# Performance work log

Measured on AMD Instinct MI355X. Metric: run time of the kernel, lower is better.

Reference implementation:

```python
import jax, jax.numpy as jnp
import numpy as np

N, C, H, W = 8, 256, 128, 128
HD = 256          # hidden_depth
FC, FS, CS = 8, 2, 8  # heads_count, fold_size, center_size
EPS_GN = 1e-5


def setup_inputs() -> dict:
    key = jax.random.key(0)
    ks = jax.random.split(key, 8)
    d = {
        'x': jax.random.normal(ks[0], (N, C, H, W), jnp.float32),
        'proj_w': jax.random.normal(ks[1], (2 * HD, C), jnp.float32) * 0.02,
        'proj_b': jnp.zeros((2 * HD,), jnp.float32),
        'merge_w': jax.random.normal(ks[2], (C, HD), jnp.float32) * 0.02,
        'merge_b': jnp.zeros((C,), jnp.float32),
        'alpha': jnp.ones((1,), jnp.float32),
        'beta': jnp.zeros((1,), jnp.float32),
        'g0_w': jnp.ones((C,), jnp.float32),
        'g0_b': jnp.zeros((C,), jnp.float32),
        'mlp_w0': jax.random.normal(ks[3], (2 * C, 2 * C), jnp.float32) * 0.02,
        'mlp_b0': jnp.zeros((2 * C,), jnp.float32),
        'mlp_w1': jax.random.normal(ks[4], (2 * C, C), jnp.float32) * 0.02,
        'mlp_b1': jnp.zeros((C,), jnp.float32),
        'g1_w': jnp.ones((C,), jnp.float32),
        'g1_b': jnp.zeros((C,), jnp.float32),
        'layer_scale': jnp.full((C,), 1e-5, jnp.float32),
    }
    return d


def _group_norm1(x, w, b):
    # GroupNorm(1, C): normalize over (C,H,W) per sample, per-channel affine
    mu = x.mean(axis=(1, 2, 3), keepdims=True)
    var = ((x - mu) ** 2).mean(axis=(1, 2, 3), keepdims=True)
    xn = (x - mu) * jax.lax.rsqrt(var + EPS_GN)
    return xn * w[None, :, None, None] + b[None, :, None, None]


def _l2norm(v):
    return v / jnp.maximum(jnp.linalg.norm(v, axis=-1, keepdims=True), 1e-12)


def _local_cluster(x, proj_w, proj_b, merge_w, merge_b, alpha, beta):
    n = x.shape[0]
    # 1x1 conv proj: C -> 2*HD
    y = jnp.einsum('nchw,oc->nohw', x, proj_w) + proj_b[None, :, None, None]
    c = y.shape[1] // FC              # per-head channels (2*HD/FC)
    h, w = H // FS, W // FS
    # 'n (fc c) (fh h) (fw w) -> (n fc fh fw) c h w'
    y = y.reshape(n, FC, c, FS, h, FS, w).transpose(0, 1, 3, 5, 2, 4, 6)
    y = y.reshape(n * FC * FS * FS, c, h, w)
    m = y.shape[0]
    # adaptive avg pool to CSxCS (h,w divisible by CS -> uniform pooling)
    center = y.reshape(m, c, CS, h // CS, CS, w // CS).mean(axis=(3, 5))
    L, s = h * w, CS * CS
    yf = y.reshape(m, c, L).transpose(0, 2, 1)       # [m, L, c]
    cf = center.reshape(m, c, s).transpose(0, 2, 1)  # [m, s, c]
    cv = c // 2
    x_point, x_value = yf[..., :cv], yf[..., cv:]
    c_point, c_value = cf[..., :cv], cf[..., cv:]
    sim = jnp.einsum('mlc,msc->mls', _l2norm(x_point), _l2norm(c_point))
    sim = jax.nn.sigmoid(alpha * sim + beta)         # [m, L, s]
    vals = sim.max(axis=2)                           # [m, L]
    idx = sim.argmax(axis=2) + s * jnp.arange(m)[:, None]
    vals = vals.reshape(-1)
    idx = idx.reshape(-1)
    xv = x_value.reshape(-1, cv)
    cvv = c_value.reshape(-1, cv)
    xv_aug = jnp.concatenate([xv, jnp.ones((xv.shape[0], 1), xv.dtype)], axis=1)
    cv_aug = jnp.concatenate([cvv, jnp.ones((cvv.shape[0], 1), cvv.dtype)], axis=1)
    # scatter-add weighted points into centers
    nc = cv_aug.at[idx].add(vals[:, None] * xv_aug)
    nc = nc[:, :-1] / nc[:, -1:]
    # gather back
    nx = vals[:, None] * nc[idx]                     # [m*L, cv]
    # '(n fc fh fw h w) c -> n (fc c) (fh h) (fw w)'
    nx = nx.reshape(n, FC, FS, FS, h, w, cv).transpose(0, 1, 6, 2, 4, 3, 5)
    nx = nx.reshape(n, FC * cv, H, W)                # [n, HD, H, W]
    return jnp.einsum('nchw,oc->nohw', nx, merge_w) + merge_b[None, :, None, None]


def reference(x, proj_w, proj_b, merge_w, merge_b, alpha, beta, g0_w, g0_b,
              mlp_w0, mlp_b0, mlp_w1, mlp_b1, g1_w, g1_b, layer_scale):
    new_x = _local_cluster(x, proj_w, proj_b, merge_w, merge_b, alpha, beta)
    new_x = _group_norm1(new_x, g0_w, g0_b)
    t = jnp.concatenate([x, new_x], axis=1)          # [n, 2C, H, W]
    t = t.transpose(0, 2, 3, 1)                      # NHWC
    t = jax.nn.gelu(t @ mlp_w0 + mlp_b0, approximate=False)
    t = t @ mlp_w1 + mlp_b1
    t = t.transpose(0, 3, 1, 2)                      # NCHW
    t = _group_norm1(t, g1_w, g1_b)
    t = t * layer_scale[None, :, None, None]
    return t + x
```

## Files before the change

kernel.cpp:

```cpp
#include <hip/hip_runtime.h>
#include <math.h>

#define PIX   16384
#define NB    8
#define CIN   256

typedef __attribute__((ext_vector_type(8))) short    short8;
typedef __attribute__((ext_vector_type(4))) float    f32x4;
typedef __attribute__((ext_vector_type(4))) unsigned short us4;
typedef __attribute__((ext_vector_type(8))) unsigned short us8;

__device__ __forceinline__ float bf2f(unsigned short h) {
  return __uint_as_float(((unsigned int)h) << 16);
}
__device__ __forceinline__ unsigned short f2bf(float f) {
  unsigned int u = __float_as_uint(f);
  return (unsigned short)((u + 0x7FFFu + ((u >> 16) & 1u)) >> 16);
}
__device__ __forceinline__ float gelu_f(float v) {
  return 0.5f * v * (1.f + erff(v * 0.70710678118654752f));
}

__device__ __forceinline__ float rowmax16(float v) {
  v = fmaxf(v, __uint_as_float(__builtin_amdgcn_update_dpp(
        __float_as_uint(v), __float_as_uint(v), 0x121, 0xF, 0xF, false)));
  v = fmaxf(v, __uint_as_float(__builtin_amdgcn_update_dpp(
        __float_as_uint(v), __float_as_uint(v), 0x122, 0xF, 0xF, false)));
  v = fmaxf(v, __uint_as_float(__builtin_amdgcn_update_dpp(
        __float_as_uint(v), __float_as_uint(v), 0x124, 0xF, 0xF, false)));
  v = fmaxf(v, __uint_as_float(__builtin_amdgcn_update_dpp(
        __float_as_uint(v), __float_as_uint(v), 0x128, 0xF, 0xF, false)));
  return v;
}

__global__ void zero_kernel(float* p, int n) {
  int i = blockIdx.x * blockDim.x + threadIdx.x;
  if (i < n) p[i] = 0.f;
}

__global__ void prep_weights(const float* __restrict__ pw_f, const float* __restrict__ mw_f,
                             const float* __restrict__ w0, const float* __restrict__ w1,
                             unsigned short* __restrict__ pw, unsigned short* __restrict__ mw,
                             unsigned short* __restrict__ w0t, unsigned short* __restrict__ w1t) {
  const int S1 = 512 * 256, S2 = 256 * 256, S3 = 512 * 512, S4 = 256 * 512;
  int i = blockIdx.x * 256 + threadIdx.x;
  if (i < S1) { pw[i] = f2bf(pw_f[i]); return; }
  i -= S1;
  if (i < S2) { mw[i] = f2bf(mw_f[i]); return; }
  i -= S2;
  if (i < S3) { int o = i >> 9, k = i & 511; w0t[i] = f2bf(w0[k * 512 + o]); return; }
  i -= S3;
  if (i < S4) { int o = i >> 9, k = i & 511; w1t[i] = f2bf(w1[k * 256 + o]); }
}

__global__ __launch_bounds__(256) void x_to_nhwc(const float* __restrict__ x,
                                                 unsigned short* __restrict__ xT) {
  __shared__ float tile[64][65];
  const int t = threadIdx.x;
  const int p0 = blockIdx.x * 64, c0 = blockIdx.y * 64, n = blockIdx.z;
#pragma unroll
  for (int i = 0; i < 4; i++) {
    const int c = i * 16 + (t >> 4);
    const float4 v = *(const float4*)(x + ((size_t)(n * 256 + c0 + c) << 14) + p0 + (t & 15) * 4);
    tile[c][(t & 15) * 4]     = v.x;
    tile[c][(t & 15) * 4 + 1] = v.y;
    tile[c][(t & 15) * 4 + 2] = v.z;
    tile[c][(t & 15) * 4 + 3] = v.w;
  }
  __syncthreads();
#pragma unroll
  for (int i = 0; i < 4; i++) {
    const int pp = i * 16 + (t >> 4);
    const int cl = (t & 15) * 4;
    us4 o;
    o.x = f2bf(tile[cl][pp]); o.y = f2bf(tile[cl + 1][pp]);
    o.z = f2bf(tile[cl + 2][pp]); o.w = f2bf(tile[cl + 3][pp]);
    *(us4*)&xT[(((size_t)n << 14) + p0 + pp) * 256 + c0 + cl] = o;
  }
}

template<bool CONCAT, bool GELU, bool STATS>
__global__ __launch_bounds__(256, 2) void mfma_gemm(
    const unsigned short* __restrict__ A, const float* __restrict__ bias,
    const unsigned short* __restrict__ B1, const unsigned short* __restrict__ B2,
    unsigned short* __restrict__ Y, int M, int K, int K1,
    int astride, int bstride, float* __restrict__ sums) {
  __shared__ unsigned short As[8192];
  __shared__ unsigned short Bs[8192];
  __shared__ float r1[4], r2[4];
  const int t = threadIdx.x;
  const int lane = t & 63, w = t >> 6;
  const int quad = lane >> 4, l16 = lane & 15;
  const int p0 = blockIdx.x * 128, m0 = blockIdx.y * 128;
  const int n = blockIdx.z;
  const int wm = w & 1, wn = w >> 1;
  const int K2 = K - K1;

  A += (size_t)n * astride;

  f32x4 acc[4][4];
#pragma unroll
  for (int im = 0; im < 4; im++)
#pragma unroll
    for (int in = 0; in < 4; in++) acc[im][in] = (f32x4)0.f;

  for (int k0 = 0; k0 < K; k0 += 64) {
    __syncthreads();
#pragma unroll
    for (int i = 0; i < 4; i++) {
      const int c = (w << 2) | i;
      const int tm = c >> 1, kk = c & 1;
      const int krow = k0 + kk * 32 + quad * 8;
      const unsigned short* ga = A + (size_t)(m0 + tm * 16 + l16) * K + krow;
      __builtin_amdgcn_global_load_lds((const __attribute__((address_space(1))) void*)ga,
          (__attribute__((address_space(3))) void*)&As[c * 512], 16, 0, 0);
      const int prow = p0 + tm * 16 + l16;
      const unsigned short* gb;
      if (!CONCAT || krow < K1)
        gb = B1 + ((((size_t)n << 14) + prow) * (size_t)K1) + krow;
      else
        gb = B2 + ((((size_t)n << 14) + prow) * (size_t)K2) + (krow - K1);
      __builtin_amdgcn_global_load_lds((const __attribute__((address_space(1))) void*)gb,
          (__attribute__((address_space(3))) void*)&Bs[c * 512], 16, 0, 0);
    }
    __syncthreads();
#pragma unroll
    for (int kk = 0; kk < 2; kk++) {
      short8 af[4], bfr[4];
#pragma unroll
      for (int im = 0; im < 4; im++)
        af[im] = *(const short8*)&As[(((wm * 4 + im) * 2 + kk) * 64 + lane) * 8];
#pragma unroll
      for (int in = 0; in < 4; in++)
        bfr[in] = *(const short8*)&Bs[(((wn * 4 + in) * 2 + kk) * 64 + lane) * 8];
#pragma unroll
      for (int im = 0; im < 4; im++)
#pragma unroll
        for (int in = 0; in < 4; in++)
          acc[im][in] = __builtin_amdgcn_mfma_f32_16x16x32_bf16(af[im], bfr[in], acc[im][in], 0, 0, 0);
    }
  }

  const size_t nb = ((size_t)n << 14);
  float s = 0.f, s2 = 0.f;
#pragma unroll
  for (int im = 0; im < 4; im++) {
    const int om = m0 + (wm * 4 + im) * 16 + quad * 4;
    const f32x4 bv = *(const f32x4*)(bias + (size_t)n * bstride + om);
#pragma unroll
    for (int in = 0; in < 4; in++) {
      const int p = p0 + (wn * 4 + in) * 16 + l16;
      float v0 = acc[im][in].x + bv.x;
      float v1 = acc[im][in].y + bv.y;
      float v2 = acc[im][in].z + bv.z;
      float v3 = acc[im][in].w + bv.w;
      if (GELU) { v0 = gelu_f(v0); v1 = gelu_f(v1); v2 = gelu_f(v2); v3 = gelu_f(v3); }
      if (STATS) {
        s += (v0 + v1) + (v2 + v3);
        s2 = fmaf(v0, v0, s2); s2 = fmaf(v1, v1, s2);
        s2 = fmaf(v2, v2, s2); s2 = fmaf(v3, v3, s2);
      }
      us4 o4;
      o4.x = f2bf(v0); o4.y = f2bf(v1); o4.z = f2bf(v2); o4.w = f2bf(v3);
      *(us4*)&Y[(nb + p) * M + om] = o4;
    }
  }
  if (STATS) {
#pragma unroll
    for (int off = 32; off > 0; off >>= 1) {
      s += __shfl_down(s, off);
      s2 += __shfl_down(s2, off);
    }
    if (lane == 0) { r1[w] = s; r2[w] = s2; }
    __syncthreads();
    if (t == 0) {
      atomicAdd(&sums[2 * n],     (r1[0] + r1[1]) + (r1[2] + r1[3]));
      atomicAdd(&sums[2 * n + 1], (r2[0] + r2[1]) + (r2[2] + r2[3]));
    }
  }
}

__global__ __launch_bounds__(1024, 4) void cluster_kernel(
    const unsigned short* __restrict__ y, const float* __restrict__ alpha_p,
    const float* __restrict__ beta_p, unsigned short* __restrict__ nx) {
  const int m = blockIdx.x;
  const int n = m >> 5, f = (m >> 2) & 7, s1 = (m >> 1) & 1, s2 = m & 1;
  const int t = threadIdx.x;
  const int wave = t >> 6, lane = t & 63;
  const int quad = lane >> 4, l16 = lane & 15;
  const float alpha = alpha_p[0], beta = beta_p[0];

  __shared__ float cs[64][68];
  __shared__ unsigned short cpnh[64][32];
  __shared__ float accv[64][36];
  __shared__ float svals[4096];
  __shared__ unsigned char sbest[4096];

  const size_t nbase = ((size_t)n << 14);
  const int prow0 = s1 * 64, pcol0 = s2 * 64;
  const int ch0 = f * 64;

  {
    const int b = t >> 4, tid = t & 15;
    const int cg = tid & 7, ph = tid >> 3;
    const int pr0 = prow0 + (b >> 3) * 8 + ph * 4;
    const int pc0 = pcol0 + (b & 7) * 8;
    const unsigned short* yb = y + (nbase + (size_t)pr0 * 128 + pc0) * 512 + ch0 + cg * 8;
    float a8[8] = {0.f, 0.f, 0.f, 0.f, 0.f, 0.f, 0.f, 0.f};
#pragma unroll
    for (int r = 0; r < 4; r++) {
      us8 buf[8];
#pragma unroll
      for (int cc = 0; cc < 8; cc++)
        buf[cc] = *(const us8*)(yb + ((size_t)r * 128 + cc) * 512);
#pragma unroll
      for (int cc = 0; cc < 8; cc++)
#pragma unroll
        for (int j = 0; j < 8; j++) a8[j] += bf2f(buf[cc][j]);
    }
#pragma unroll
    for (int j = 0; j < 8; j++) a8[j] += __shfl_xor(a8[j], 8);
    if (ph == 0) {
      f32x4 o0, o1;
      o0.x = a8[0] * (1.f / 64.f); o0.y = a8[1] * (1.f / 64.f);
      o0.z = a8[2] * (1.f / 64.f); o0.w = a8[3] * (1.f / 64.f);
      o1.x = a8[4] * (1.f / 64.f); o1.y = a8[5] * (1.f / 64.f);
      o1.z = a8[6] * (1.f / 64.f); o1.w = a8[7] * (1.f / 64.f);
      *(f32x4*)&cs[b][cg * 8]     = o0;
      *(f32x4*)&cs[b][cg * 8 + 4] = o1;
    }
  }
  __syncthreads();

  if (t < 64) {
    const int b = t;
    float s = 0.f;
#pragma unroll
    for (int cc = 0; cc < 32; cc++) { float v = cs[b][cc]; s = fmaf(v, v, s); }
    const float inv = 1.f / fmaxf(sqrtf(s), 1e-12f);
#pragma unroll
    for (int cc = 0; cc < 32; cc++) cpnh[b][cc] = f2bf(cs[b][cc] * inv);
#pragma unroll
    for (int q = 0; q < 32; q++) accv[b][q] = cs[b][32 + q];
    accv[b][32] = 1.f;
  }
  __syncthreads();

  const short8 cb0 = *(const short8*)&cpnh[ 0 + l16][quad * 8];
  const short8 cb1 = *(const short8*)&cpnh[16 + l16][quad * 8];
  const short8 cb2 = *(const short8*)&cpnh[32 + l16][quad * 8];
  const short8 cb3 = *(const short8*)&cpnh[48 + l16][quad * 8];
  const int sl4 = (((l16 >> 2) << 4) | (l16 & 3)) << 2;
  const int sh = quad << 4;

  auto loadpt = [&](int tile, short8& a, short8& v) {
    const int pidx = wave * 256 + tile * 16;
    const int pix = (prow0 + (pidx >> 6)) * 128 + pcol0 + (pidx & 63) + l16;
    const unsigned short* yp = y + (nbase + pix) * 512 + ch0 + quad * 8;
    a = *(const short8*)yp;
    v = *(const short8*)(yp + 32);
  };

  auto compute_tile = [&](int tile, short8 apt, short8 avl) {
    const int pidx = wave * 256 + tile * 16;

    float nrm = 0.f;
#pragma unroll
    for (int j = 0; j < 8; j++) {
      const float fv = bf2f((unsigned short)apt[j]);
      nrm = fmaf(fv, fv, nrm);
    }
    nrm += __shfl_xor(nrm, 16);
    nrm += __shfl_xor(nrm, 32);
    const float inva = 1.f / fmaxf(sqrtf(nrm), 1e-12f);

    const f32x4 d0 = __builtin_amdgcn_mfma_f32_16x16x32_bf16(apt, cb0, (f32x4)0.f, 0, 0, 0);
    const f32x4 d1 = __builtin_amdgcn_mfma_f32_16x16x32_bf16(apt, cb1, (f32x4)0.f, 0, 0, 0);
    const f32x4 d2 = __builtin_amdgcn_mfma_f32_16x16x32_bf16(apt, cb2, (f32x4)0.f, 0, 0, 0);
    const f32x4 d3 = __builtin_amdgcn_mfma_f32_16x16x32_bf16(apt, cb3, (f32x4)0.f, 0, 0, 0);

    float bv[4]; int bi[4];
#pragma unroll
    for (int r = 0; r < 4; r++) {
      float v = fmaxf(fmaxf(d0[r], d1[r]), fmaxf(d2[r], d3[r]));
      v = rowmax16(v);
      bv[r] = v;
      const unsigned long long m0 = __ballot(d0[r] == v);
      const unsigned long long m1 = __ballot(d1[r] == v);
      const unsigned long long m2 = __ballot(d2[r] == v);
      const unsigned long long m3 = __ballot(d3[r] == v);
      const unsigned f0 = (unsigned)(m0 >> sh) & 0xFFFFu;
      const unsigned f1 = (unsigned)(m1 >> sh) & 0xFFFFu;
      const unsigned f2 = (unsigned)(m2 >> sh) & 0xFFFFu;
      const unsigned f3 = (unsigned)(m3 >> sh) & 0xFFFFu;
      int ii = 48 + __ffs(f3) - 1;
      if (f2) ii = 32 + __ffs(f2) - 1;
      if (f1) ii = 16 + __ffs(f1) - 1;
      if (f0) ii = __ffs(f0) - 1;
      bi[r] = ii;
    }

    const float rv01 = (l16 & 1) ? bv[1] : bv[0];
    const float rv23 = (l16 & 1) ? bv[3] : bv[2];
    const float rowv = (l16 & 2) ? rv23 : rv01;
    const int   ri01 = (l16 & 1) ? bi[1] : bi[0];
    const int   ri23 = (l16 & 1) ? bi[3] : bi[2];
    const int   rowi = (l16 & 2) ? ri23 : ri01;
    const unsigned pk = (__float_as_uint(rowv) & ~63u) | (unsigned)rowi;
    const unsigned got = (unsigned)__builtin_amdgcn_ds_bpermute(sl4, (int)pk);
    const int   idx = (int)(got & 63u);
    const float dot = __uint_as_float(got & ~63u);

    const float val = 1.f / (1.f + __expf(-fmaf(alpha, dot * inva, beta)));
    if (quad == 0) {
      svals[pidx + l16] = val;
      sbest[pidx + l16] = (unsigned char)idx;
    }
#pragma unroll
    for (int j = 0; j < 8; j++)
      atomicAdd(&accv[idx][quad * 8 + j], val * bf2f((unsigned short)avl[j]));
    if (quad == 0) atomicAdd(&accv[idx][32], val);
  };

  {
    short8 aA, vA, aB, vB, aC, vC, aD, vD;
    short8 nA = {}, wA = {}, nB = {}, wB = {};
    short8 nC = {}, wC = {}, nD = {}, wD = {};
    loadpt(0, aA, vA); loadpt(1, aB, vB); loadpt(2, aC, vC); loadpt(3, aD, vD);
#pragma unroll 1
    for (int tp = 0; tp < 16; tp += 4) {
      if (tp < 12) {
        loadpt(tp + 4, nA, wA); loadpt(tp + 5, nB, wB);
        loadpt(tp + 6, nC, wC); loadpt(tp + 7, nD, wD);
      }
      compute_tile(tp,     aA, vA);
      compute_tile(tp + 1, aB, vB);
      compute_tile(tp + 2, aC, vC);
      compute_tile(tp + 3, aD, vD);
      if (tp < 12) {
        aA = nA; vA = wA; aB = nB; vB = wB;
        aC = nC; vC = wC; aD = nD; vD = wD;
      }
    }
  }
  __syncthreads();

  for (int i = t; i < 2048; i += 1024) {
    const int b = i >> 5, q = i & 31;
    accv[b][q] = accv[b][q] / accv[b][32];
  }
  __syncthreads();

#pragma unroll
  for (int i = 0; i < 4; i++) {
    const int l = i * 1024 + t;
    const int p = (prow0 + (l >> 6)) * 128 + pcol0 + (l & 63);
    const float v = svals[l];
    const int b = sbest[l];
    unsigned short* nr = nx + (nbase + p) * 256 + f * 32;
#pragma unroll
    for (int q8 = 0; q8 < 4; q8++) {
      const f32x4 a0 = *(const f32x4*)&accv[b][q8 * 8];
      const f32x4 a1 = *(const f32x4*)&accv[b][q8 * 8 + 4];
      us8 o;
      o[0] = f2bf(v * a0.x); o[1] = f2bf(v * a0.y);
      o[2] = f2bf(v * a0.z); o[3] = f2bf(v * a0.w);
      o[4] = f2bf(v * a1.x); o[5] = f2bf(v * a1.y);
      o[6] = f2bf(v * a1.z); o[7] = f2bf(v * a1.w);
      *(us8*)&nr[q8 * 8] = o;
    }
  }
}

__global__ void gn_finalize0(const float* __restrict__ sums, const float* __restrict__ g0w,
                             const float* __restrict__ g0b, float* __restrict__ scl,
                             float* __restrict__ bia) {
  const int n = blockIdx.x, c = threadIdx.x;
  const float cntinv = 1.f / (float)(CIN * PIX);
  const float mu = sums[2 * n] * cntinv;
  const float var = sums[2 * n + 1] * cntinv - mu * mu;
  const float rs = rsqrtf(var + 1e-5f);
  const float a = rs * g0w[c];
  scl[n * 256 + c] = a;
  bia[n * 256 + c] = g0b[c] - mu * a;
}

__global__ void w0_scale(const unsigned short* __restrict__ w0t,
                         const float* __restrict__ scl, unsigned short* __restrict__ w0s) {
  const int n = blockIdx.y;
  const int i = blockIdx.x * 256 + threadIdx.x;
  const int k = i & 511;
  unsigned short v = w0t[i];
  if (k >= 256) v = f2bf(bf2f(v) * scl[n * 256 + k - 256]);
  w0s[(size_t)n * 262144 + i] = v;
}

__global__ void b0_eff(const unsigned short* __restrict__ w0t, const float* __restrict__ b0,
                       const float* __restrict__ bia, float* __restrict__ b0e) {
  const int n = blockIdx.y;
  const int o = blockIdx.x * 256 + threadIdx.x;
  float s = b0[o];
  const unsigned short* wr = w0t + (size_t)o * 512 + 256;
  const float* br = bia + n * 256;
#pragma unroll 4
  for (int k = 0; k < 256; k++) s = fmaf(bf2f(wr[k]), br[k], s);
  b0e[n * 512 + o] = s;
}

__global__ __launch_bounds__(256) void final_transpose(
    const unsigned short* __restrict__ u, const float* __restrict__ x,
    const float* __restrict__ sums, const float* __restrict__ g1w,
    const float* __restrict__ g1b, const float* __restrict__ lsc,
    float* __restrict__ out) {
  __shared__ float tile[64][68];
  const int t = threadIdx.x;
  const int p0 = blockIdx.x * 64, c0 = blockIdx.y * 64, n = blockIdx.z;
  {
    const int pl = t >> 2, g = t & 3;
    const unsigned short* up = u + ((((size_t)n << 14) + p0 + pl) << 8) + c0 + g * 16;
    const us8 v0 = *(const us8*)up;
    const us8 v1 = *(const us8*)(up + 8);
#pragma unroll
    for (int j = 0; j < 8; j++) {
      tile[pl][g * 16 + j] = bf2f(v0[j]);
      tile[pl][g * 16 + 8 + j] = bf2f(v1[j]);
    }
  }
  __syncthreads();
  {
    const int cl = t >> 2, g = t & 3;
    const int c = c0 + cl;
    const float cntinv = 1.f / (float)(CIN * PIX);
    const float mu = sums[2 * n] * cntinv;
    const float var = sums[2 * n + 1] * cntinv - mu * mu;
    const float rs = rsqrtf(var + 1e-5f);
    const float gw = rs * g1w[c] * lsc[c];
    const float gb = (g1b[c] - mu * rs * g1w[c]) * lsc[c];
    const size_t rowb = ((size_t)(n * 256 + c) << 14) + p0 + g * 16;
#pragma unroll
    for (int q = 0; q < 4; q++) {
      const float4 xv = *(const float4*)(x + rowb + q * 4);
      float4 o;
      o.x = fmaf(tile[g * 16 + q * 4][cl], gw, gb) + xv.x;
      o.y = fmaf(tile[g * 16 + q * 4 + 1][cl], gw, gb) + xv.y;
      o.z = fmaf(tile[g * 16 + q * 4 + 2][cl], gw, gb) + xv.z;
      o.w = fmaf(tile[g * 16 + q * 4 + 3][cl], gw, gb) + xv.w;
      *(float4*)(out + rowb + q * 4) = o;
    }
  }
}

extern "C" void kernel_launch(void* const* d_in, const int* in_sizes, int n_in,
                              void* d_out, int out_size, void* d_ws, size_t ws_size,
                              hipStream_t stream) {
  const float* x       = (const float*)d_in[0];
  const float* proj_w  = (const float*)d_in[1];
  const float* proj_b  = (const float*)d_in[2];
  const float* merge_w = (const float*)d_in[3];
  const float* merge_b = (const float*)d_in[4];
  const float* alpha   = (const float*)d_in[5];
  const float* beta    = (const float*)d_in[6];
  const float* g0w     = (const float*)d_in[7];
  const float* g0b     = (const float*)d_in[8];
  const float* w0      = (const float*)d_in[9];
  const float* b0      = (const float*)d_in[10];
  const float* w1      = (const float*)d_in[11];
  const float* b1      = (const float*)d_in[12];
  const float* g1w     = (const float*)d_in[13];
  const float* g1b     = (const float*)d_in[14];
  const float* lsc     = (const float*)d_in[15];
  float* out = (float*)d_out;

  unsigned short* wsu = (unsigned short*)d_ws;
  unsigned short* xT  = wsu;
  unsigned short* y   = xT + (size_t)33554432;
  unsigned short* nx  = y + (size_t)67108864;
  unsigned short* pw  = nx + (size_t)33554432;
  unsigned short* mw  = pw + 131072;
  unsigned short* w0t = mw + 65536;
  unsigned short* w1t = w0t + 262144;
  unsigned short* w0s = w1t + 131072;
  float* sums = (float*)(w0s + (size_t)2097152);
  float* scl0 = sums + 32;
  float* bia0 = scl0 + 2048;
  float* b0e  = bia0 + 2048;
  unsigned short* newx = (unsigned short*)d_out;

  zero_kernel<<<1, 64, 0, stream>>>(sums, 32);
  prep_weights<<<2304, 256, 0, stream>>>(proj_w, merge_w, w0, w1, pw, mw, w0t, w1t);
  x_to_nhwc<<<dim3(256, 4, NB), 256, 0, stream>>>(x, xT);

  mfma_gemm<false, false, false><<<dim3(128, 4, NB), 256, 0, stream>>>(
      pw, proj_b, xT, nullptr, y, 512, 256, 256, 0, 0, nullptr);

  cluster_kernel<<<256, 1024, 0, stream>>>(y, alpha, beta, nx);

  mfma_gemm<false, false, true><<<dim3(128, 2, NB), 256, 0, stream>>>(
      mw, merge_b, nx, nullptr, newx, 256, 256, 256, 0, 0, sums);

  gn_finalize0<<<NB, 256, 0, stream>>>(sums, g0w, g0b, scl0, bia0);
  w0_scale<<<dim3(1024, NB), 256, 0, stream>>>(w0t, scl0, w0s);
  b0_eff<<<dim3(2, NB), 256, 0, stream>>>(w0t, b0, bia0, b0e);

  mfma_gemm<true, true, false><<<dim3(128, 4, NB), 256, 0, stream>>>(
      w0s, b0e, xT, newx, y, 512, 512, 256, 262144, 512, nullptr);

  mfma_gemm<false, false, true><<<dim3(128, 2, NB), 256, 0, stream>>>(
      w1t, b1, y, nullptr, nx, 256, 512, 512, 0, 0, sums + 16);

  final_transpose<<<dim3(256, 4, NB), 256, 0, stream>>>(
      nx, x, sums + 16, g1w, g1b, lsc, out);
}
```

Baseline: 977.8 us.

## Split cluster kernel into centers, assign and gather kernels across slices

Replaces the single 256-block cluster kernel with three kernels: one computes pooled centers, one assigns points and accumulates per-slice partial sums, and one reduces the partials and scatters the results. Each cluster is now spread across 8 blocks, so the grid has far more blocks than the old 256 and fills the GPU better. The cost is extra global-memory traffic for the intermediates (centers, values, best indices, partial sums), two extra kernel launches, and scratch space carved out of the output buffer.

```diff
diff --git a/kernel.cpp b/kernel.cpp
--- a/kernel.cpp
+++ b/kernel.cpp
@@ -180,29 +180,22 @@
   }
 }
 
-__global__ __launch_bounds__(1024, 4) void cluster_kernel(
-    const unsigned short* __restrict__ y, const float* __restrict__ alpha_p,
-    const float* __restrict__ beta_p, unsigned short* __restrict__ nx) {
-  const int m = blockIdx.x;
+
+__global__ __launch_bounds__(256) void centers_kernel(
+    const unsigned short* __restrict__ y, unsigned short* __restrict__ cpnh_g,
+    float* __restrict__ cval_g) {
+  const int m = blockIdx.y, slice = blockIdx.x;
   const int n = m >> 5, f = (m >> 2) & 7, s1 = (m >> 1) & 1, s2 = m & 1;
   const int t = threadIdx.x;
-  const int wave = t >> 6, lane = t & 63;
-  const int quad = lane >> 4, l16 = lane & 15;
-  const float alpha = alpha_p[0], beta = beta_p[0];
-
-  __shared__ float cs[64][68];
-  __shared__ unsigned short cpnh[64][32];
-  __shared__ float accv[64][36];
-  __shared__ float svals[4096];
-  __shared__ unsigned char sbest[4096];
+  __shared__ float cs[16][68];
 
   const size_t nbase = ((size_t)n << 14);
-  const int prow0 = s1 * 64, pcol0 = s2 * 64;
-  const int ch0 = f * 64;
+  const int prow0 = s1 * 64, pcol0 = s2 * 64, ch0 = f * 64;
 
   {
-    const int b = t >> 4, tid = t & 15;
-    const int cg = tid & 7, ph = tid >> 3;
+    const int bl = t >> 4;
+    const int b = slice * 16 + bl;
+    const int tid = t & 15, cg = tid & 7, ph = tid >> 3;
     const int pr0 = prow0 + (b >> 3) * 8 + ph * 4;
     const int pc0 = pcol0 + (b & 7) * 8;
     const unsigned short* yb = y + (nbase + (size_t)pr0 * 128 + pc0) * 512 + ch0 + cg * 8;
@@ -226,35 +219,61 @@
       o0.z = a8[2] * (1.f / 64.f); o0.w = a8[3] * (1.f / 64.f);
       o1.x = a8[4] * (1.f / 64.f); o1.y = a8[5] * (1.f / 64.f);
       o1.z = a8[6] * (1.f / 64.f); o1.w = a8[7] * (1.f / 64.f);
-      *(f32x4*)&cs[b][cg * 8]     = o0;
-      *(f32x4*)&cs[b][cg * 8 + 4] = o1;
+      *(f32x4*)&cs[bl][cg * 8]     = o0;
+      *(f32x4*)&cs[bl][cg * 8 + 4] = o1;
     }
   }
   __syncthreads();
 
-  if (t < 64) {
-    const int b = t;
+  if (t < 128) {
+    const int bl = t >> 3, jg = t & 7;
+    const int bg = slice * 16 + bl;
+    if (jg < 8) {
+      f32x4 ov;
+      ov.x = cs[bl][32 + jg * 4]; ov.y = cs[bl][32 + jg * 4 + 1];
+      ov.z = cs[bl][32 + jg * 4 + 2]; ov.w = cs[bl][32 + jg * 4 + 3];
+      *(f32x4*)&cval_g[((size_t)(m * 64 + bg) << 5) + jg * 4] = ov;
+    }
     float s = 0.f;
 #pragma unroll
-    for (int cc = 0; cc < 32; cc++) { float v = cs[b][cc]; s = fmaf(v, v, s); }
+    for (int cc = 0; cc < 32; cc++) { const float v = cs[bl][cc]; s = fmaf(v, v, s); }
     const float inv = 1.f / fmaxf(sqrtf(s), 1e-12f);
-#pragma unroll
-    for (int cc = 0; cc < 32; cc++) cpnh[b][cc] = f2bf(cs[b][cc] * inv);
-#pragma unroll
-    for (int q = 0; q < 32; q++) accv[b][q] = cs[b][32 + q];
-    accv[b][32] = 1.f;
-  }
-  __syncthreads();
-
-  const short8 cb0 = *(const short8*)&cpnh[ 0 + l16][quad * 8];
-  const short8 cb1 = *(const short8*)&cpnh[16 + l16][quad * 8];
-  const short8 cb2 = *(const short8*)&cpnh[32 + l16][quad * 8];
-  const short8 cb3 = *(const short8*)&cpnh[48 + l16][quad * 8];
+    us4 o;
+    o.x = f2bf(cs[bl][jg * 4] * inv);     o.y = f2bf(cs[bl][jg * 4 + 1] * inv);
+    o.z = f2bf(cs[bl][jg * 4 + 2] * inv); o.w = f2bf(cs[bl][jg * 4 + 3] * inv);
+    *(us4*)&cpnh_g[((size_t)(m * 64 + bg) << 5) + jg * 4] = o;
+  }
+}
+
+__global__ __launch_bounds__(256, 8) void assign_kernel(
+    const unsigned short* __restrict__ y, const unsigned short* __restrict__ cpnh_g,
+    const float* __restrict__ alpha_p, const float* __restrict__ beta_p,
+    float* __restrict__ svals_g, unsigned char* __restrict__ sbest_g,
+    float* __restrict__ accp_v, float* __restrict__ accp_c) {
+  const int m = blockIdx.y, slice = blockIdx.x;
+  const int n = m >> 5, f = (m >> 2) & 7, s1 = (m >> 1) & 1, s2 = m & 1;
+  const int t = threadIdx.x;
+  const int wave = t >> 6, lane = t & 63;
+  const int quad = lane >> 4, l16 = lane & 15;
+  const float alpha = alpha_p[0], beta = beta_p[0];
+
+  __shared__ float accv[64][34];
+
+  for (int i = t; i < 64 * 34; i += 256) ((float*)accv)[i] = 0.f;
+
+  const size_t nbase = ((size_t)n << 14);
+  const int prow0 = s1 * 64, pcol0 = s2 * 64, ch0 = f * 64;
+
+  const short8 cb0 = *(const short8*)&cpnh_g[((size_t)(m * 64 +  0 + l16) << 5) + quad * 8];
+  const short8 cb1 = *(const short8*)&cpnh_g[((size_t)(m * 64 + 16 + l16) << 5) + quad * 8];
+  const short8 cb2 = *(const short8*)&cpnh_g[((size_t)(m * 64 + 32 + l16) << 5) + quad * 8];
+  const short8 cb3 = *(const short8*)&cpnh_g[((size_t)(m * 64 + 48 + l16) << 5) + quad * 8];
   const int sl4 = (((l16 >> 2) << 4) | (l16 & 3)) << 2;
   const int sh = quad << 4;
+  __syncthreads();
 
   auto loadpt = [&](int tile, short8& a, short8& v) {
-    const int pidx = wave * 256 + tile * 16;
+    const int pidx = slice * 512 + wave * 128 + tile * 16;
     const int pix = (prow0 + (pidx >> 6)) * 128 + pcol0 + (pidx & 63) + l16;
     const unsigned short* yp = y + (nbase + pix) * 512 + ch0 + quad * 8;
     a = *(const short8*)yp;
@@ -262,7 +281,7 @@
   };
 
   auto compute_tile = [&](int tile, short8 apt, short8 avl) {
-    const int pidx = wave * 256 + tile * 16;
+    const int pidx = slice * 512 + wave * 128 + tile * 16;
 
     float nrm = 0.f;
 #pragma unroll
@@ -313,8 +332,8 @@
 
     const float val = 1.f / (1.f + __expf(-fmaf(alpha, dot * inva, beta)));
     if (quad == 0) {
-      svals[pidx + l16] = val;
-      sbest[pidx + l16] = (unsigned char)idx;
+      svals_g[(size_t)m * 4096 + pidx + l16] = val;
+      sbest_g[(size_t)m * 4096 + pidx + l16] = (unsigned char)idx;
     }
 #pragma unroll
     for (int j = 0; j < 8; j++)
@@ -323,50 +342,69 @@
   };
 
   {
-    short8 aA, vA, aB, vB, aC, vC, aD, vD;
-    short8 nA = {}, wA = {}, nB = {}, wB = {};
-    short8 nC = {}, wC = {}, nD = {}, wD = {};
-    loadpt(0, aA, vA); loadpt(1, aB, vB); loadpt(2, aC, vC); loadpt(3, aD, vD);
+    short8 a0, v0, a1 = {}, v1 = {};
+    loadpt(0, a0, v0);
 #pragma unroll 1
-    for (int tp = 0; tp < 16; tp += 4) {
-      if (tp < 12) {
-        loadpt(tp + 4, nA, wA); loadpt(tp + 5, nB, wB);
-        loadpt(tp + 6, nC, wC); loadpt(tp + 7, nD, wD);
-      }
-      compute_tile(tp,     aA, vA);
-      compute_tile(tp + 1, aB, vB);
-      compute_tile(tp + 2, aC, vC);
-      compute_tile(tp + 3, aD, vD);
-      if (tp < 12) {
-        aA = nA; vA = wA; aB = nB; vB = wB;
-        aC = nC; vC = wC; aD = nD; vD = wD;
-      }
+    for (int tp = 0; tp < 8; tp++) {
+      if (tp < 7) loadpt(tp + 1, a1, v1);
+      compute_tile(tp, a0, v0);
+      a0 = a1; v0 = v1;
     }
   }
   __syncthreads();
 
-  for (int i = t; i < 2048; i += 1024) {
+  const size_t pb = ((size_t)(m * 8 + slice)) * 64;
+  for (int i = t; i < 2048; i += 256) {
     const int b = i >> 5, q = i & 31;
-    accv[b][q] = accv[b][q] / accv[b][32];
+    accp_v[(pb + b) * 32 + q] = accv[b][q];
+  }
+  if (t < 64) accp_c[pb + t] = accv[t][32];
+}
+
+__global__ __launch_bounds__(256) void gather_kernel(
+    const float* __restrict__ accp_v, const float* __restrict__ accp_c,
+    const float* __restrict__ cval_g, const float* __restrict__ svals_g,
+    const unsigned char* __restrict__ sbest_g, unsigned short* __restrict__ nx) {
+  const int m = blockIdx.y, slice = blockIdx.x;
+  const int n = m >> 5, f = (m >> 2) & 7, s1 = (m >> 1) & 1, s2 = m & 1;
+  const int t = threadIdx.x;
+  __shared__ float cm[64][34];
+
+  const size_t nbase = ((size_t)n << 14);
+  const int prow0 = s1 * 64, pcol0 = s2 * 64;
+
+  for (int i = t; i < 2048; i += 256) {
+    const int b = i >> 5, q = i & 31;
+    float s = cval_g[((size_t)(m * 64 + b) << 5) + q];
+    float c = 1.f;
+#pragma unroll
+    for (int s8 = 0; s8 < 8; s8++) {
+      const size_t pb = ((size_t)(m * 8 + s8)) * 64 + b;
+      s += accp_v[pb * 32 + q];
+      c += accp_c[pb];
+    }
+    cm[b][q] = s / c;
   }
   __syncthreads();
 
 #pragma unroll
-  for (int i = 0; i < 4; i++) {
-    const int l = i * 1024 + t;
+  for (int pass = 0; pass < 2; pass++) {
+    const int l = slice * 512 + pass * 256 + t;
     const int p = (prow0 + (l >> 6)) * 128 + pcol0 + (l & 63);
-    const float v = svals[l];
-    const int b = sbest[l];
+    const float v = svals_g[(size_t)m * 4096 + l];
+    const int b = sbest_g[(size_t)m * 4096 + l];
     unsigned short* nr = nx + (nbase + p) * 256 + f * 32;
 #pragma unroll
     for (int q8 = 0; q8 < 4; q8++) {
-      const f32x4 a0 = *(const f32x4*)&accv[b][q8 * 8];
-      const f32x4 a1 = *(const f32x4*)&accv[b][q8 * 8 + 4];
+      const float2 a0 = *(const float2*)&cm[b][q8 * 8];
+      const float2 a1 = *(const float2*)&cm[b][q8 * 8 + 2];
+      const float2 a2 = *(const float2*)&cm[b][q8 * 8 + 4];
+      const float2 a3 = *(const float2*)&cm[b][q8 * 8 + 6];
       us8 o;
       o[0] = f2bf(v * a0.x); o[1] = f2bf(v * a0.y);
-      o[2] = f2bf(v * a0.z); o[3] = f2bf(v * a0.w);
-      o[4] = f2bf(v * a1.x); o[5] = f2bf(v * a1.y);
-      o[6] = f2bf(v * a1.z); o[7] = f2bf(v * a1.w);
+      o[2] = f2bf(v * a1.x); o[3] = f2bf(v * a1.y);
+      o[4] = f2bf(v * a2.x); o[5] = f2bf(v * a2.y);
+      o[6] = f2bf(v * a3.x); o[7] = f2bf(v * a3.y);
       *(us8*)&nr[q8 * 8] = o;
     }
   }
@@ -486,6 +524,13 @@
   float* b0e  = bia0 + 2048;
   unsigned short* newx = (unsigned short*)d_out;
 
+  float* svals_g = (float*)((char*)d_out + 67108864);
+  float* cval_g  = svals_g + 1048576;
+  float* accp_v  = cval_g + 524288;
+  float* accp_c  = accp_v + 4194304;
+  unsigned short* cpnh_g = (unsigned short*)(accp_c + 131072);
+  unsigned char*  sbest_g = (unsigned char*)(cpnh_g + 524288);
+
   zero_kernel<<<1, 64, 0, stream>>>(sums, 32);
   prep_weights<<<2304, 256, 0, stream>>>(proj_w, merge_w, w0, w1, pw, mw, w0t, w1t);
   x_to_nhwc<<<dim3(256, 4, NB), 256, 0, stream>>>(x, xT);
@@ -493,7 +538,11 @@
   mfma_gemm<false, false, false><<<dim3(128, 4, NB), 256, 0, stream>>>(
       pw, proj_b, xT, nullptr, y, 512, 256, 256, 0, 0, nullptr);
 
-  cluster_kernel<<<256, 1024, 0, stream>>>(y, alpha, beta, nx);
+  centers_kernel<<<dim3(4, 256), 256, 0, stream>>>(y, cpnh_g, cval_g);
+  assign_kernel<<<dim3(8, 256), 256, 0, stream>>>(
+      y, cpnh_g, alpha, beta, svals_g, sbest_g, accp_v, accp_c);
+  gather_kernel<<<dim3(8, 256), 256, 0, stream>>>(
+      accp_v, accp_c, cval_g, svals_g, sbest_g, nx);
 
   mfma_gemm<false, false, true><<<dim3(128, 2, NB), 256, 0, stream>>>(
       mw, merge_b, nx, nullptr, newx, 256, 256, 256, 0, 0, sums);
```

Measured after the change: 1.007 ms. 1.03x slower.
